# Kernel optimization log

Hardware: AMD Instinct MI355X
Metric: run time of the kernel (lower is better)

## Reference

```python
import jax, jax.numpy as jnp
import numpy as np

N = 64        # SSM state size
L = 262144    # l_max / sequence length


def setup_inputs() -> dict:
    key = jax.random.key(0)
    ks = jax.random.split(key, 8)
    u = jax.random.normal(ks[0], (L,), dtype=jnp.float32)
    # HiPPO-DPLR style eigenvalue init
    Lambda_re = -0.5 * jnp.ones((N,), jnp.float32)
    Lambda_im = jnp.pi * jnp.arange(N, dtype=jnp.float32)
    P_re = jax.random.normal(ks[1], (N,), jnp.float32)
    P_im = jax.random.normal(ks[2], (N,), jnp.float32)
    B_re = jax.random.normal(ks[3], (N,), jnp.float32)
    B_im = jax.random.normal(ks[4], (N,), jnp.float32)
    C_ri = (0.5 ** 0.5) * jax.random.normal(ks[5], (N, 2), jnp.float32)  # C = C_ri[:,0] + i*C_ri[:,1]
    D = jnp.ones((1,), jnp.float32)
    log_step = jax.random.uniform(ks[6], (1,), jnp.float32,
                                  minval=float(np.log(0.001)), maxval=float(np.log(0.1)))
    return {"u": u, "Lambda_re": Lambda_re, "Lambda_im": Lambda_im,
            "P_re": P_re, "P_im": P_im, "B_re": B_re, "B_im": B_im,
            "C_ri": C_ri, "D": D, "log_step": log_step}


def _kernel_DPLR(Lambda, P, Q, B, C, step, l):
    # Evaluate the SSM generating function at the l roots of unity (bilinear discretization)
    Omega = jnp.exp((-2j * jnp.pi) * (jnp.arange(l) / l))          # (L,)
    g = (2.0 / step) * ((1.0 - Omega) / (1.0 + Omega))             # (L,)
    c = 2.0 / (1.0 + Omega)                                        # (L,)
    # Core Cauchy matrix: the single large (L, N) complex intermediate
    recip = 1.0 / (g[:, None] - Lambda[None, :])                   # (L, N)
    # Four Cauchy dot products fused into one thin matmul
    v = jnp.stack([C.conj() * B, C.conj() * P,
                   Q.conj() * B, Q.conj() * P], axis=1)            # (N, 4)
    k = recip @ v                                                  # (L, 4)
    k00, k01, k10, k11 = k[:, 0], k[:, 1], k[:, 2], k[:, 3]
    atRoots = c * (k00 - k01 * (1.0 / (1.0 + k11)) * k10)          # (L,)
    return jnp.fft.ifft(atRoots, l).real                           # (L,) real kernel


def _causal_convolution(u, K):
    l = u.shape[0]
    ud = jnp.fft.rfft(jnp.pad(u, (0, K.shape[0])))
    Kd = jnp.fft.rfft(jnp.pad(K, (0, l)))
    return jnp.fft.irfft(ud * Kd)[:l]


def reference(u, Lambda_re, Lambda_im, P_re, P_im, B_re, B_im, C_ri, D, log_step):
    Lambda = Lambda_re + 1j * Lambda_im
    P = P_re + 1j * P_im
    B = B_re + 1j * B_im
    C = C_ri[:, 0] + 1j * C_ri[:, 1]
    step = jnp.exp(log_step)                                       # (1,)
    K = _kernel_DPLR(Lambda, P, P, B, C, step, u.shape[0])
    return _causal_convolution(u, K) + D * u
```

## Files before the change

kernel.cpp:

```cpp
#include <hip/hip_runtime.h>
#include <math.h>

#define L_LEN  262144
#define NST    64
#define TPB    256
#define PI2F   6.2831853071795864769f
#define PIF    3.1415926535897932385f

__device__ inline float2 cmul(float2 a, float2 b) {
    return make_float2(a.x*b.x - a.y*b.y, a.x*b.y + a.y*b.x);
}

template<int M, int NF>
__device__ float2* lds_fft_r4(float2* b0, float2* b1, float sgn) {
    float2* src = b0; float2* dst = b1;
    int Ns = 1;
    while (Ns * 4 <= M) {
        __syncthreads();
        const int NB = NF * (M / 4);
        for (int bi = threadIdx.x; bi < NB; bi += TPB) {
            int f = bi / (M / 4);
            int j = bi & (M / 4 - 1);
            int r = j & (Ns - 1);
            const float2* s = src + f * M;
            float2 x0 = s[j];
            float2 x1 = s[j +     (M/4)];
            float2 x2 = s[j + 2 * (M/4)];
            float2 x3 = s[j + 3 * (M/4)];
            float ang = sgn * PI2F * ((float)r / (float)(4 * Ns));
            float sn, cs; __sincosf(ang, &sn, &cs);
            float2 w1 = make_float2(cs, sn);
            float2 w2 = cmul(w1, w1);
            float2 w3 = cmul(w2, w1);
            x1 = cmul(x1, w1); x2 = cmul(x2, w2); x3 = cmul(x3, w3);
            float2 t0 = make_float2(x0.x + x2.x, x0.y + x2.y);
            float2 t1 = make_float2(x0.x - x2.x, x0.y - x2.y);
            float2 t2 = make_float2(x1.x + x3.x, x1.y + x3.y);
            float2 t3 = make_float2(x1.x - x3.x, x1.y - x3.y);
            float2* d = dst + f * M + ((j - r) << 2) + r;
            d[0]      = make_float2(t0.x + t2.x, t0.y + t2.y);
            d[Ns]     = make_float2(t1.x - sgn * t3.y, t1.y + sgn * t3.x);
            d[2 * Ns] = make_float2(t0.x - t2.x, t0.y - t2.y);
            d[3 * Ns] = make_float2(t1.x + sgn * t3.y, t1.y - sgn * t3.x);
        }
        float2* t = src; src = dst; dst = t;
        Ns <<= 2;
    }
    if (Ns < M) {
        __syncthreads();
        const int NB = NF * (M / 2);
        for (int bi = threadIdx.x; bi < NB; bi += TPB) {
            int f = bi / (M / 2);
            int j = bi & (M / 2 - 1);
            const float2* s = src + f * M;
            float2 a = s[j];
            float2 b = s[j + M / 2];
            float ang = sgn * PI2F * ((float)j / (float)M);
            float sn, cs; __sincosf(ang, &sn, &cs);
            float2 wb = make_float2(cs * b.x - sn * b.y, cs * b.y + sn * b.x);
            float2* d = dst + f * M + j;
            d[0]     = make_float2(a.x + wb.x, a.y + wb.y);
            d[M / 2] = make_float2(a.x - wb.x, a.y - wb.y);
        }
        float2* t = src; src = dst; dst = t;
    }
    __syncthreads();
    return src;
}


__global__ __launch_bounds__(TPB) void k1_pass1(
    const float* __restrict__ u,
    const float* __restrict__ Lre, const float* __restrict__ Lim,
    const float* __restrict__ Pre, const float* __restrict__ Pim,
    const float* __restrict__ Bre, const float* __restrict__ Bim,
    const float* __restrict__ Cri,
    float2* __restrict__ T_U, float2* __restrict__ T_Uo,
    float4* __restrict__ tab)
{
    __shared__ float2 b0[1024], b1[1024];
    const int t = threadIdx.x, bx = blockIdx.x;
    const int sig = bx & 1;
    const int c0  = bx & 510;
    const float invL = 1.0f / (float)L_LEN;
    if (bx == 0 && t < NST) {
        float lr = Lre[t], li = Lim[t];
        float pr = Pre[t], pi = Pim[t];
        float br = Bre[t], bi = Bim[t];
        float cr = Cri[2*t], ci = Cri[2*t+1];
        float dx = -lr;
        float v00x = cr*br + ci*bi, v00y = cr*bi - ci*br;
        float v01x = cr*pr + ci*pi, v01y = cr*pi - ci*pr;
        float v10x = pr*br + pi*bi, v10y = pr*bi - pi*br;
        float v11x = pr*pr + pi*pi;
        tab[t]       = make_float4(li, dx*dx, dx*v11x, -v11x);
        tab[t + 64]  = make_float4(dx*v00x, v00y, dx*v00y, -v00x);
        tab[t + 128] = make_float4(dx*v01x, v01y, dx*v01y, -v01x);
        tab[t + 192] = make_float4(dx*v10x, v10y, dx*v10y, -v10x);
    }
    for (int i = t; i < 1024; i += TPB) {
        int f = i & 1, e = i >> 1;
        int n = (c0 + f) + (e << 9);
        float uv = u[n];
        if (sig) {
            float sn, cs; __sincosf(PIF * ((float)n * invL), &sn, &cs);
            b0[(f << 9) + e] = make_float2(uv * cs, -uv * sn);
        } else {
            b0[(f << 9) + e] = make_float2(uv, 0.f);
        }
    }
    float2* r = lds_fft_r4<512, 2>(b0, b1, -1.f);
    float2* Tout = sig ? T_Uo : T_U;
    for (int i = t; i < 1024; i += TPB) {
        int f = i & 1, k = i >> 1;
        int c = c0 + f;
        float ang = -PI2F * ((float)(c * k) * invL);
        float sn, cs; __sincosf(ang, &sn, &cs);
        Tout[(k << 9) + c] = cmul(make_float2(cs, sn), r[(f << 9) + k]);
    }
}

__global__ __launch_bounds__(TPB) void k2_spectral(
    const float2* __restrict__ T_U, const float2* __restrict__ T_Uo,
    const float4* __restrict__ tab, const float* __restrict__ lstp,
    float2* __restrict__ T_Ve, float2* __restrict__ T_Vo)
{
    __shared__ float2 b0[1024], b1[1024];
    const int t = threadIdx.x, m1 = blockIdx.x;
    const float invL = 1.0f / (float)L_LEN;
    for (int i = t; i < 1024; i += TPB) {
        int f = i >> 9, e = i & 511;
        const float2* Tin = f ? T_Uo : T_U;
        b0[i] = Tin[(m1 << 9) + e];
    }
    float2* r = lds_fft_r4<512, 2>(b0, b1, -1.f);
    float2* o = (r == b0) ? b1 : b0;

    float G2 = 2.0f / expf(lstp[0]);
    float tn[4], gi[4], acc[4][8];
    #pragma unroll
    for (int p = 0; p < 4; ++p) {
        int k1 = t + ((p & 1) << 8);
        float jf = (float)(m1 + (k1 << 9)) + ((p & 2) ? 0.5f : 0.0f);
        float h = PIF * (jf * invL);
        float sn, cs; __sincosf(h, &sn, &cs);
        float tv = sn * __frcp_rn(cs);
        tv = fminf(fmaxf(tv, -1e7f), 1e7f);
        tn[p] = tv; gi[p] = G2 * tv;
        #pragma unroll
        for (int q = 0; q < 8; ++q) acc[p][q] = 0.f;
    }
    #pragma unroll 4
    for (int n = 0; n < NST; ++n) {
        float4 a  = tab[n];
        float4 b  = tab[n + 64];
        float4 cc = tab[n + 128];
        float4 d  = tab[n + 192];
        #pragma unroll
        for (int p = 0; p < 4; ++p) {
            float dy   = gi[p] - a.x;
            float iv   = __frcp_rn(fmaf(dy, dy, a.y));
            float ivdy = iv * dy;
            acc[p][6] = fmaf(iv, a.z, acc[p][6]);
            acc[p][7] = fmaf(ivdy, a.w, acc[p][7]);
            acc[p][0] = fmaf(iv, b.x,  fmaf(ivdy, b.y,  acc[p][0]));
            acc[p][1] = fmaf(iv, b.z,  fmaf(ivdy, b.w,  acc[p][1]));
            acc[p][2] = fmaf(iv, cc.x, fmaf(ivdy, cc.y, acc[p][2]));
            acc[p][3] = fmaf(iv, cc.z, fmaf(ivdy, cc.w, acc[p][3]));
            acc[p][4] = fmaf(iv, d.x,  fmaf(ivdy, d.y,  acc[p][4]));
            acc[p][5] = fmaf(iv, d.z,  fmaf(ivdy, d.w,  acc[p][5]));
        }
    }
    #pragma unroll
    for (int p = 0; p < 4; ++p) {
        int k1 = t + ((p & 1) << 8);
        float ax = 1.f + acc[p][6], ay = acc[p][7];
        float im = 1.f / (ax*ax + ay*ay);
        float tx = acc[p][2]*acc[p][4] - acc[p][3]*acc[p][5];
        float ty = acc[p][2]*acc[p][5] + acc[p][3]*acc[p][4];
        float wx = acc[p][0] - (tx*ax + ty*ay) * im;
        float wy = acc[p][1] - (ty*ax - tx*ay) * im;
        float2 H = make_float2(wx - tn[p]*wy, wy + tn[p]*wx);
        if (p & 2) o[512 + k1] = cmul(r[512 + k1], H);
        else       o[k1]       = cmul(r[k1],       H);
    }
    float2* r2 = lds_fft_r4<512, 2>(o, r, +1.f);
    for (int i = t; i < 1024; i += TPB) {
        int v = i >> 9, j = i & 511;
        float ang = PI2F * ((float)(m1 * j) * invL);
        float sn, cs; __sincosf(ang, &sn, &cs);
        float2 val = cmul(make_float2(cs, sn), r2[(v << 9) + j]);
        if (v == 0) T_Ve[(j << 9) + m1] = val;
        else        T_Vo[(j << 9) + m1] = val;
    }
}

__global__ __launch_bounds__(TPB) void k3_out(
    const float2* __restrict__ T_Ve, const float2* __restrict__ T_Vo,
    const float* __restrict__ u, const float* __restrict__ Dp,
    float* __restrict__ out)
{
    __shared__ float2 b0[1024], b1[1024];
    const int t = threadIdx.x, j = blockIdx.x;
    const float invL = 1.0f / (float)L_LEN;
    for (int i = t; i < 512; i += TPB) {
        b0[i]       = T_Ve[(j << 9) + i];
        b0[i + 512] = T_Vo[(j << 9) + i];
    }
    float2* r = lds_fft_r4<512, 2>(b0, b1, +1.f);
    const float sc = 0.5f * invL;
    const float D = Dp[0];
    for (int p = t; p < 512; p += TPB) {
        int n = j + (p << 9);
        float sn, cs; __sincosf(PIF * ((float)n * invL), &sn, &cs);
        float2 yE = r[p];
        float2 yO = r[p + 512];
        out[n] = fmaf(D, u[n], (yE.x + cs * yO.x - sn * yO.y) * sc);
    }
}

extern "C" void kernel_launch(void* const* d_in, const int* in_sizes, int n_in,
                              void* d_out, int out_size, void* d_ws, size_t ws_size,
                              hipStream_t stream) {
    const float* u    = (const float*)d_in[0];
    const float* Lre  = (const float*)d_in[1];
    const float* Lim  = (const float*)d_in[2];
    const float* Pre  = (const float*)d_in[3];
    const float* Pim  = (const float*)d_in[4];
    const float* Bre  = (const float*)d_in[5];
    const float* Bim  = (const float*)d_in[6];
    const float* Cri  = (const float*)d_in[7];
    const float* Dp   = (const float*)d_in[8];
    const float* lstp = (const float*)d_in[9];
    float* out = (float*)d_out;

    char* ws = (char*)d_ws;
    float2* T_U  = (float2*)(ws);
    float2* T_Uo = (float2*)(ws + (2u << 20));
    float2* T_Ve = (float2*)(ws + (4u << 20));
    float2* T_Vo = (float2*)(ws + (6u << 20));
    float4* tab  = (float4*)(ws + (8u << 20));

    k1_pass1   <<<512, TPB, 0, stream>>>(u, Lre,Lim,Pre,Pim,Bre,Bim,Cri,
                                         T_U, T_Uo, tab);
    k2_spectral<<<512, TPB, 0, stream>>>(T_U, T_Uo, tab, lstp, T_Ve, T_Vo);
    k3_out     <<<512, TPB, 0, stream>>>(T_Ve, T_Vo, u, Dp, out);
}
```

Measured before the change: 118.5 us.

## Pack two real columns per complex FFT in pass one; pair accumulators as float2

The first pass now packs two real input columns into one complex FFT and separates them afterwards with the conjugate-symmetry trick. The odd (half-shifted) signal is formed from the same packed data via a pre-twiddle. This halves the number of blocks and FFTs in k1 at the cost of an extra unpacking step with mirrored LDS reads. Separately, the Cauchy accumulation in k2 is regrouped into float2 fma pairs, which may let the compiler emit packed FMA instructions.

```diff
diff --git a/kernel.cpp b/kernel.cpp
--- a/kernel.cpp
+++ b/kernel.cpp
@@ -9,6 +9,9 @@
 
 __device__ inline float2 cmul(float2 a, float2 b) {
     return make_float2(a.x*b.x - a.y*b.y, a.x*b.y + a.y*b.x);
+}
+__device__ inline float2 f2fma(float2 a, float2 b, float2 c) {
+    return make_float2(fmaf(a.x, b.x, c.x), fmaf(a.y, b.y, c.y));
 }
 
 template<int M, int NF>
@@ -80,8 +83,7 @@
 {
     __shared__ float2 b0[1024], b1[1024];
     const int t = threadIdx.x, bx = blockIdx.x;
-    const int sig = bx & 1;
-    const int c0  = bx & 510;
+    const int c0 = bx << 1;
     const float invL = 1.0f / (float)L_LEN;
     if (bx == 0 && t < NST) {
         float lr = Lre[t], li = Lim[t];
@@ -98,25 +100,26 @@
         tab[t + 128] = make_float4(dx*v01x, v01y, dx*v01y, -v01x);
         tab[t + 192] = make_float4(dx*v10x, v10y, dx*v10y, -v10x);
     }
-    for (int i = t; i < 1024; i += TPB) {
-        int f = i & 1, e = i >> 1;
-        int n = (c0 + f) + (e << 9);
-        float uv = u[n];
-        if (sig) {
-            float sn, cs; __sincosf(PIF * ((float)n * invL), &sn, &cs);
-            b0[(f << 9) + e] = make_float2(uv * cs, -uv * sn);
-        } else {
-            b0[(f << 9) + e] = make_float2(uv, 0.f);
-        }
+    for (int e = t; e < 512; e += TPB) {
+        float2 z0 = make_float2(u[c0 + (e << 9)], u[c0 + 1 + (e << 9)]);
+        b0[e] = z0;
+        float sn, cs; __sincosf(PIF * ((float)e * (1.0f / 512.f)), &sn, &cs);
+        b0[512 + e] = cmul(z0, make_float2(cs, -sn));
     }
     float2* r = lds_fft_r4<512, 2>(b0, b1, -1.f);
-    float2* Tout = sig ? T_Uo : T_U;
-    for (int i = t; i < 1024; i += TPB) {
-        int f = i & 1, k = i >> 1;
+    for (int i = t; i < 2048; i += TPB) {
+        int sig = i >> 10, f = i & 1, k = (i >> 1) & 511;
+        int mir = sig ? (511 - k) : ((512 - k) & 511);
+        float2 Zk = r[(sig << 9) + k];
+        float2 Zm = r[(sig << 9) + mir];
+        float2 Y = f ? make_float2(0.5f * (Zk.y + Zm.y), 0.5f * (Zm.x - Zk.x))
+                     : make_float2(0.5f * (Zk.x + Zm.x), 0.5f * (Zk.y - Zm.y));
         int c = c0 + f;
-        float ang = -PI2F * ((float)(c * k) * invL);
-        float sn, cs; __sincosf(ang, &sn, &cs);
-        Tout[(k << 9) + c] = cmul(make_float2(cs, sn), r[(f << 9) + k]);
+        float num = sig ? (float)(c * ((k << 1) + 1)) : (float)((c * k) << 1);
+        float sn, cs; __sincosf(-PIF * (num * invL), &sn, &cs);
+        float2 val = cmul(make_float2(cs, sn), Y);
+        if (sig) T_Uo[(k << 9) + c] = val;
+        else     T_U [(k << 9) + c] = val;
     }
 }
 
@@ -137,7 +140,8 @@
     float2* o = (r == b0) ? b1 : b0;
 
     float G2 = 2.0f / expf(lstp[0]);
-    float tn[4], gi[4], acc[4][8];
+    float tn[4], gi[4];
+    float2 K00[4], K01[4], K10[4], K11[4];
     #pragma unroll
     for (int p = 0; p < 4; ++p) {
         int k1 = t + ((p & 1) << 8);
@@ -147,8 +151,8 @@
         float tv = sn * __frcp_rn(cs);
         tv = fminf(fmaxf(tv, -1e7f), 1e7f);
         tn[p] = tv; gi[p] = G2 * tv;
-        #pragma unroll
-        for (int q = 0; q < 8; ++q) acc[p][q] = 0.f;
+        K00[p] = make_float2(0.f, 0.f); K01[p] = make_float2(0.f, 0.f);
+        K10[p] = make_float2(0.f, 0.f); K11[p] = make_float2(0.f, 0.f);
     }
     #pragma unroll 4
     for (int n = 0; n < NST; ++n) {
@@ -161,25 +165,25 @@
             float dy   = gi[p] - a.x;
             float iv   = __frcp_rn(fmaf(dy, dy, a.y));
             float ivdy = iv * dy;
-            acc[p][6] = fmaf(iv, a.z, acc[p][6]);
-            acc[p][7] = fmaf(ivdy, a.w, acc[p][7]);
-            acc[p][0] = fmaf(iv, b.x,  fmaf(ivdy, b.y,  acc[p][0]));
-            acc[p][1] = fmaf(iv, b.z,  fmaf(ivdy, b.w,  acc[p][1]));
-            acc[p][2] = fmaf(iv, cc.x, fmaf(ivdy, cc.y, acc[p][2]));
-            acc[p][3] = fmaf(iv, cc.z, fmaf(ivdy, cc.w, acc[p][3]));
-            acc[p][4] = fmaf(iv, d.x,  fmaf(ivdy, d.y,  acc[p][4]));
-            acc[p][5] = fmaf(iv, d.z,  fmaf(ivdy, d.w,  acc[p][5]));
+            float2 vi = make_float2(iv, iv), vd = make_float2(ivdy, ivdy);
+            K11[p] = f2fma(make_float2(iv, ivdy), make_float2(a.z, a.w), K11[p]);
+            K00[p] = f2fma(vi, make_float2(b.x,  b.z),
+                     f2fma(vd, make_float2(b.y,  b.w),  K00[p]));
+            K01[p] = f2fma(vi, make_float2(cc.x, cc.z),
+                     f2fma(vd, make_float2(cc.y, cc.w), K01[p]));
+            K10[p] = f2fma(vi, make_float2(d.x,  d.z),
+                     f2fma(vd, make_float2(d.y,  d.w),  K10[p]));
         }
     }
     #pragma unroll
     for (int p = 0; p < 4; ++p) {
         int k1 = t + ((p & 1) << 8);
-        float ax = 1.f + acc[p][6], ay = acc[p][7];
+        float ax = 1.f + K11[p].x, ay = K11[p].y;
         float im = 1.f / (ax*ax + ay*ay);
-        float tx = acc[p][2]*acc[p][4] - acc[p][3]*acc[p][5];
-        float ty = acc[p][2]*acc[p][5] + acc[p][3]*acc[p][4];
-        float wx = acc[p][0] - (tx*ax + ty*ay) * im;
-        float wy = acc[p][1] - (ty*ax - tx*ay) * im;
+        float tx = K01[p].x*K10[p].x - K01[p].y*K10[p].y;
+        float ty = K01[p].x*K10[p].y + K01[p].y*K10[p].x;
+        float wx = K00[p].x - (tx*ax + ty*ay) * im;
+        float wy = K00[p].y - (ty*ax - tx*ay) * im;
         float2 H = make_float2(wx - tn[p]*wy, wy + tn[p]*wx);
         if (p & 2) o[512 + k1] = cmul(r[512 + k1], H);
         else       o[k1]       = cmul(r[k1],       H);
@@ -241,7 +245,7 @@
     float2* T_Vo = (float2*)(ws + (6u << 20));
     float4* tab  = (float4*)(ws + (8u << 20));
 
-    k1_pass1   <<<512, TPB, 0, stream>>>(u, Lre,Lim,Pre,Pim,Bre,Bim,Cri,
+    k1_pass1   <<<256, TPB, 0, stream>>>(u, Lre,Lim,Pre,Pim,Bre,Bim,Cri,
                                          T_U, T_Uo, tab);
     k2_spectral<<<512, TPB, 0, stream>>>(T_U, T_Uo, tab, lstp, T_Ve, T_Vo);
     k3_out     <<<512, TPB, 0, stream>>>(T_Ve, T_Vo, u, Dp, out);
```

Result: no change. 117.8 us (-0.6%).
